# Performance work log

Hardware: AMD Instinct MI355X
Metric: run time of the kernel (lower is better)

## Reference

```python
import jax, jax.numpy as jnp
import numpy as np

DIM = 2048
NH = 16
NKV = 4
HD = DIM // NH  # 128
ROPE_BASE = 10000.0
QK_GAIN_INIT = 1.0


def setup_inputs() -> dict:
    key = jax.random.key(0)
    ks = jax.random.split(key, 6)
    kv_dim = NKV * HD
    s = 0.02
    return {
        "x": jax.random.normal(ks[0], (2, 2048, DIM), dtype=jnp.float32),
        "wq": jax.random.normal(ks[1], (DIM, DIM), dtype=jnp.float32) * s,
        "wk": jax.random.normal(ks[2], (kv_dim, DIM), dtype=jnp.float32) * s,
        "wv": jax.random.normal(ks[3], (kv_dim, DIM), dtype=jnp.float32) * s,
        "wproj": jax.random.normal(ks[4], (DIM, DIM), dtype=jnp.float32) * s,
        "q_gain": jnp.full((NH,), QK_GAIN_INIT, dtype=jnp.float32),
    }


def _rms_norm(t):
    eps = jnp.asarray(jnp.finfo(t.dtype).eps, t.dtype)
    ms = jnp.mean(jnp.square(t), axis=-1, keepdims=True)
    return t * jax.lax.rsqrt(ms + eps)


def _rope_tables(seqlen, dtype):
    inv_freq = 1.0 / (ROPE_BASE ** (np.arange(0, HD, 2, dtype=np.float32) / HD))
    t = np.arange(seqlen, dtype=np.float32)
    freqs = np.outer(t, inv_freq)  # [S, HD/2]
    cos = jnp.asarray(np.cos(freqs), dtype=dtype)[None, None]  # [1,1,S,HD/2]
    sin = jnp.asarray(np.sin(freqs), dtype=dtype)[None, None]
    return cos, sin


def _apply_rotary(x, cos, sin):
    half = x.shape[-1] // 2
    x1, x2 = x[..., :half], x[..., half:]
    return jnp.concatenate((x1 * cos + x2 * sin, -x1 * sin + x2 * cos), axis=-1)


def reference(x, wq, wk, wv, wproj, q_gain):
    B, S, D = x.shape
    # projections (torch F.linear: x @ W.T), reshape to [B, H, S, HD]
    q = (x @ wq.T).reshape(B, S, NH, HD).transpose(0, 2, 1, 3)
    k = (x @ wk.T).reshape(B, S, NKV, HD).transpose(0, 2, 1, 3)
    v = (x @ wv.T).reshape(B, S, NKV, HD).transpose(0, 2, 1, 3)
    q = _rms_norm(q)
    k = _rms_norm(k)
    cos, sin = _rope_tables(S, q.dtype)
    q = _apply_rotary(q, cos, sin)
    k = _apply_rotary(k, cos, sin)
    q = q * q_gain.astype(q.dtype)[None, :, None, None]
    # GQA: expand kv heads
    G = NH // NKV
    k = jnp.repeat(k, G, axis=1)  # [B, NH, S, HD]
    v = jnp.repeat(v, G, axis=1)
    scale = 1.0 / np.sqrt(HD)
    scores = jnp.einsum("bhsd,bhtd->bhst", q, k) * scale
    causal = jnp.tril(jnp.ones((S, S), dtype=bool))
    scores = jnp.where(causal[None, None], scores, jnp.finfo(scores.dtype).min)
    attn = jax.nn.softmax(scores, axis=-1)
    y = jnp.einsum("bhst,bhtd->bhsd", attn, v)
    y = y.transpose(0, 2, 1, 3).reshape(B, S, D)
    return y @ wproj.T
```

## Files before the change

kernel.cpp:

```cpp
#include <hip/hip_runtime.h>
#include <hip/hip_bf16.h>
#include <stdint.h>

#define DIM 2048
#define NH 16
#define NKV 4
#define HD 128
#define BATCH 2
#define SEQ 2048

typedef unsigned short ushort_t;
typedef __attribute__((ext_vector_type(8))) short short8;
typedef __attribute__((ext_vector_type(4))) float f32x4;
typedef __attribute__((ext_vector_type(16))) float f32x16;

__device__ inline ushort_t f2b(float f) {
    union { float f; uint32_t u; } v; v.f = f;
    uint32_t r = (v.u + 0x7fffu + ((v.u >> 16) & 1u)) >> 16;
    return (ushort_t)r;
}

__device__ inline float fexp2(float x) {
#if __has_builtin(__builtin_amdgcn_exp2f)
    return __builtin_amdgcn_exp2f(x);
#else
    float r; asm("v_exp_f32 %0, %1" : "=v"(r) : "v"(x)); return r;
#endif
}

__global__ void cast_all(const float* __restrict__ x, const float* __restrict__ wq,
                         const float* __restrict__ wk, const float* __restrict__ wv,
                         const float* __restrict__ wp,
                         ushort_t* __restrict__ xb, ushort_t* __restrict__ wqkvb,
                         ushort_t* __restrict__ wprojb) {
    const int stride = gridDim.x * blockDim.x;
    for (int i = blockIdx.x * blockDim.x + threadIdx.x; i < 4718592; i += stride) {
        const float* s; ushort_t* d; int off;
        if (i < 2097152)      { s = x;  d = xb;               off = i; }
        else if (i < 3145728) { s = wq; d = wqkvb;            off = i - 2097152; }
        else if (i < 3407872) { s = wk; d = wqkvb + 4194304;  off = i - 3145728; }
        else if (i < 3670016) { s = wv; d = wqkvb + 5242880;  off = i - 3407872; }
        else                  { s = wp; d = wprojb;           off = i - 3670016; }
        float4 v = ((const float4*)s)[off];
        ushort4 o;
        o.x = f2b(v.x); o.y = f2b(v.y); o.z = f2b(v.z); o.w = f2b(v.w);
        ((ushort4*)d)[off] = o;
    }
}

__device__ inline void gload_lds16(const ushort_t* g, ushort_t* l) {
    __builtin_amdgcn_global_load_lds((const __attribute__((address_space(1))) void*)g,
                                     (__attribute__((address_space(3))) void*)l, 16, 0, 0);
}

__launch_bounds__(256, 2)
__global__ void gemm_bt(const ushort_t* __restrict__ A, const ushort_t* __restrict__ Bm,
                        float* __restrict__ C, int M, int N, int K) {
    __shared__ ushort_t lA[128 * 64];
    __shared__ ushort_t lB[128 * 64];
    const int t = threadIdx.x;
    const int lane = t & 63;
    const int w = t >> 6;
    const int wr = w >> 1, wc = w & 1;
    const int g = lane >> 4, l16 = lane & 15;
    const int nwg = gridDim.x * gridDim.y;
    const int bid = blockIdx.y * gridDim.x + blockIdx.x;
    const int cpx = nwg >> 3;
    const int swz = (bid & 7) * cpx + (bid >> 3);
    const int nbx = gridDim.x;
    const int m0 = (swz / nbx) * 128, n0 = (swz % nbx) * 128;

    f32x4 acc[4][4];
#pragma unroll
    for (int i = 0; i < 4; i++)
#pragma unroll
        for (int j = 0; j < 4; j++) acc[i][j] = (f32x4){0, 0, 0, 0};

    const int row_s = t >> 3;
    const int cx = t & 7;
    const int xr = (lane & 7);

    for (int kt = 0; kt < (K >> 6); ++kt) {
        const int k0 = kt * 64;
        __syncthreads();
#pragma unroll
        for (int i = 0; i < 4; i++) {
            const int ra = i * 32 + row_s;
            gload_lds16(A + (size_t)(m0 + ra) * K + k0 + ((cx ^ (row_s & 7)) * 8), lA + i * 2048 + t * 8);
            gload_lds16(Bm + (size_t)(n0 + ra) * K + k0 + ((cx ^ (row_s & 7)) * 8), lB + i * 2048 + t * 8);
        }
        __syncthreads();
#pragma unroll
        for (int kk = 0; kk < 2; kk++) {
            short8 af[4], bf[4];
#pragma unroll
            for (int i = 0; i < 4; i++) {
                af[i] = *(const short8*)(lA + (wr * 64 + i * 16 + l16) * 64 + (((kk * 4 + g) ^ xr) * 8));
                bf[i] = *(const short8*)(lB + (wc * 64 + i * 16 + l16) * 64 + (((kk * 4 + g) ^ xr) * 8));
            }
#pragma unroll
            for (int i = 0; i < 4; i++)
#pragma unroll
                for (int j = 0; j < 4; j++)
                    acc[i][j] = __builtin_amdgcn_mfma_f32_16x16x32_bf16(af[i], bf[j], acc[i][j], 0, 0, 0);
        }
    }
#pragma unroll
    for (int i = 0; i < 4; i++)
#pragma unroll
        for (int j = 0; j < 4; j++) {
            int rb = m0 + wr * 64 + i * 16 + g * 4;
            int cb = n0 + wc * 64 + j * 16 + l16;
#pragma unroll
            for (int r = 0; r < 4; r++)
                C[(size_t)(rb + r) * N + cb] = acc[i][j][r];
        }
}

__launch_bounds__(256, 2)
__global__ void gemm_qkv(const ushort_t* __restrict__ A, const ushort_t* __restrict__ Bm,
                         const float* __restrict__ qgain,
                         ushort_t* __restrict__ qb, ushort_t* __restrict__ kb,
                         ushort_t* __restrict__ vtb) {
    const int K = 2048;
    __shared__ ushort_t lA[128 * 64];
    __shared__ ushort_t lB[128 * 64];
    __shared__ float psum[2][128];
    const int t = threadIdx.x;
    const int lane = t & 63;
    const int w = t >> 6;
    const int wr = w >> 1, wc = w & 1;
    const int g = lane >> 4, l16 = lane & 15;
    const int nwg = gridDim.x * gridDim.y;
    const int bid = blockIdx.y * gridDim.x + blockIdx.x;
    const int cpx = nwg >> 3;
    const int swz = (bid & 7) * cpx + (bid >> 3);
    const int nt = swz % 24;
    const int m0 = (swz / 24) * 128, n0 = nt * 128;

    int cm[4];
    cm[0] = wc * 32 + l16;
    cm[1] = wc * 32 + 16 + l16;
    cm[2] = cm[0] + 64;
    cm[3] = cm[1] + 64;

    f32x4 acc[4][4];
#pragma unroll
    for (int i = 0; i < 4; i++)
#pragma unroll
        for (int j = 0; j < 4; j++) acc[i][j] = (f32x4){0, 0, 0, 0};

    const int row_s = t >> 3;
    const int cx = t & 7;
    const int xr = (lane & 7);

    for (int kt = 0; kt < (K >> 6); ++kt) {
        const int k0 = kt * 64;
        __syncthreads();
#pragma unroll
        for (int i = 0; i < 4; i++) {
            const int ra = i * 32 + row_s;
            gload_lds16(A + (size_t)(m0 + ra) * K + k0 + ((cx ^ (row_s & 7)) * 8), lA + i * 2048 + t * 8);
            gload_lds16(Bm + (size_t)(n0 + ra) * K + k0 + ((cx ^ (row_s & 7)) * 8), lB + i * 2048 + t * 8);
        }
        __syncthreads();
#pragma unroll
        for (int kk = 0; kk < 2; kk++) {
            short8 af[4], bf[4];
#pragma unroll
            for (int i = 0; i < 4; i++) {
                af[i] = *(const short8*)(lA + (wr * 64 + i * 16 + l16) * 64 + (((kk * 4 + g) ^ xr) * 8));
                bf[i] = *(const short8*)(lB + cm[i] * 64 + (((kk * 4 + g) ^ xr) * 8));
            }
#pragma unroll
            for (int i = 0; i < 4; i++)
#pragma unroll
                for (int j = 0; j < 4; j++)
                    acc[i][j] = __builtin_amdgcn_mfma_f32_16x16x32_bf16(af[i], bf[j], acc[i][j], 0, 0, 0);
        }
    }

    const int b = m0 >> 11;
    const int s0 = m0 & 2047;

    if (nt < 20) {
        float ssq[4][4];
#pragma unroll
        for (int i = 0; i < 4; i++)
#pragma unroll
            for (int r = 0; r < 4; r++) {
                float v = 0.0f;
#pragma unroll
                for (int j = 0; j < 4; j++) v += acc[i][j][r] * acc[i][j][r];
#pragma unroll
                for (int m = 1; m < 16; m <<= 1) v += __shfl_xor(v, m, 64);
                ssq[i][r] = v;
            }
        if (l16 == 0) {
#pragma unroll
            for (int i = 0; i < 4; i++)
#pragma unroll
                for (int r = 0; r < 4; r++)
                    psum[wc][wr * 64 + i * 16 + g * 4 + r] = ssq[i][r];
        }
        __syncthreads();

        const float gsc = (nt < 16) ? qgain[nt] * (0.08838834764831845f * 1.4426950408889634f)
                                    : 1.0f;
        ushort_t* outp = (nt < 16) ? qb + (size_t)(b * NH + nt) * SEQ * HD
                                   : kb + (size_t)(b * NKV + (nt - 16)) * SEQ * HD;
        const float inv0 = exp2f(-(float)cm[0] * (13.287712379549449f / 64.0f));
        const float inv1 = exp2f(-(float)cm[1] * (13.287712379549449f / 64.0f));
#pragma unroll
        for (int i = 0; i < 4; i++)
#pragma unroll
            for (int r = 0; r < 4; r++) {
                const int sloc = wr * 64 + i * 16 + g * 4 + r;
                const float tot = psum[0][sloc] + psum[1][sloc];
                const float rg = rsqrtf(tot * (1.0f / 128.0f) + 1.1920929e-07f) * gsc;
                const float fs = (float)(s0 + sloc);
                ushort_t* orow = outp + (size_t)(s0 + sloc) * HD;
#pragma unroll
                for (int jp = 0; jp < 2; jp++) {
                    float x1 = acc[i][jp][r], x2 = acc[i][jp + 2][r];
                    float sn, c;
                    __sincosf(fs * (jp ? inv1 : inv0), &sn, &c);
                    orow[cm[jp]]      = f2b((x1 * c + x2 * sn) * rg);
                    orow[cm[jp] + 64] = f2b((x2 * c - x1 * sn) * rg);
                }
            }
    } else {
        ushort_t* vout = vtb + (size_t)((b * NKV + (nt - 20)) * HD) * SEQ;
#pragma unroll
        for (int i = 0; i < 4; i++)
#pragma unroll
            for (int j = 0; j < 4; j++) {
                ushort4 o;
                o.x = f2b(acc[i][j][0]); o.y = f2b(acc[i][j][1]);
                o.z = f2b(acc[i][j][2]); o.w = f2b(acc[i][j][3]);
                *(ushort4*)(vout + (size_t)cm[j] * SEQ + s0 + wr * 64 + i * 16 + g * 4) = o;
            }
    }
}

#define KVB 64

__launch_bounds__(256, 2)
__global__ void attn(const ushort_t* __restrict__ qbuf, const ushort_t* __restrict__ kbuf,
                     const ushort_t* __restrict__ vtbuf, ushort_t* __restrict__ ybuf) {
    __shared__ ushort_t Klds[KVB * HD];
    __shared__ ushort_t Vlds[HD * KVB];

    const int idx = blockIdx.x;
    const int pass = idx >> 8;
    const int rr0 = idx & 255;
    const int xcd = rr0 & 7;
    const int jj = rr0 >> 5;
    const int qt = pass ? jj : 15 - jj;
    const int bh = xcd * 4 + ((rr0 >> 3) & 3);
    const int b = bh >> 4, hh = bh & 15;
    const int kvh = hh >> 2;
    const int t = threadIdx.x;
    const int w = t >> 6, lane = t & 63;
    const int l31 = lane & 31, hf = lane >> 5;
    const int q0 = qt * 128;
    const int qbase = q0 + w * 32;

    const ushort_t* Qp = qbuf + (size_t)(b * NH + hh) * SEQ * HD;
    const ushort_t* Kp = kbuf + (size_t)(b * NKV + kvh) * SEQ * HD;
    const ushort_t* Vtp = vtbuf + (size_t)(b * NKV + kvh) * HD * SEQ;

    short8 aq[8];
#pragma unroll
    for (int dc = 0; dc < 8; dc++)
        aq[dc] = *(const short8*)(Qp + (size_t)(qbase + l31) * HD + dc * 16 + hf * 8);

    f32x16 y[4];
#pragma unroll
    for (int db = 0; db < 4; db++)
#pragma unroll
        for (int r = 0; r < 16; r++) y[db][r] = 0.0f;
    float mrun = -1e30f, lrun = 0.0f;

    const int k_row = t >> 2;
    const int k_c0 = (t & 3) * 4;
    const int v_row = t >> 1;
    const int v_c0 = (t & 1) * 4;

    short8 kreg[4], vreg[4];
    const int ntiles = q0 / 64 + 2;

#pragma unroll
    for (int i = 0; i < 4; i++) {
        kreg[i] = *(const short8*)(Kp + (size_t)k_row * HD + (k_c0 + i) * 8);
        vreg[i] = *(const short8*)(Vtp + (size_t)v_row * SEQ + (v_c0 + i) * 8);
    }

    for (int kt = 0; kt < ntiles; ++kt) {
        const int kv0 = kt * KVB;
        __syncthreads();
        {
            ushort_t* kd = Klds + k_row * HD;
            ushort_t* vd = Vlds + v_row * KVB;
#pragma unroll
            for (int i = 0; i < 4; i++)
                *(short8*)(kd + (((k_c0 + i) ^ (k_row & 15)) * 8)) = kreg[i];
#pragma unroll
            for (int i = 0; i < 4; i++)
                *(short8*)(vd + (((v_c0 + i) ^ (v_row & 7)) * 8)) = vreg[i];
        }
        __syncthreads();
        if (kt + 1 < ntiles) {
            const int nkv0 = kv0 + KVB;
#pragma unroll
            for (int i = 0; i < 4; i++) {
                kreg[i] = *(const short8*)(Kp + (size_t)(nkv0 + k_row) * HD + (k_c0 + i) * 8);
                vreg[i] = *(const short8*)(Vtp + (size_t)v_row * SEQ + nkv0 + (v_c0 + i) * 8);
            }
        }

        if (kv0 <= qbase + 31) {
            f32x16 s0v, s1v;
#pragma unroll
            for (int r = 0; r < 16; r++) { s0v[r] = 0.0f; s1v[r] = 0.0f; }
#pragma unroll
            for (int dc = 0; dc < 8; dc++) {
                short8 ak0 = *(const short8*)(Klds + (size_t)(l31) * HD      + (((dc * 2 + hf) ^ (l31 & 15)) * 8));
                short8 ak1 = *(const short8*)(Klds + (size_t)(32 + l31) * HD + (((dc * 2 + hf) ^ (l31 & 15)) * 8));
                s0v = __builtin_amdgcn_mfma_f32_32x32x16_bf16(ak0, aq[dc], s0v, 0, 0, 0);
                s1v = __builtin_amdgcn_mfma_f32_32x32x16_bf16(ak1, aq[dc], s1v, 0, 0, 0);
            }

            const int qabs = qbase + l31;
            if (kv0 + 63 > qbase) {
#pragma unroll
                for (int r = 0; r < 16; r++) {
                    int kvr = kv0 + (r & 3) + 8 * (r >> 2) + 4 * hf;
                    if (kvr > qabs)      s0v[r] = -1e30f;
                    if (kvr + 32 > qabs) s1v[r] = -1e30f;
                }
            }

            float mt = -1e30f;
#pragma unroll
            for (int r = 0; r < 16; r++) mt = fmaxf(mt, fmaxf(s0v[r], s1v[r]));
            mt = fmaxf(mt, __shfl_xor(mt, 32, 64));
            if (!__all(mt <= mrun + 8.0f)) {
                float mn = fmaxf(mrun, mt);
                float al = fexp2(mrun - mn);
                mrun = mn;
                lrun *= al;
#pragma unroll
                for (int r = 0; r < 16; r++) {
                    float alr = __shfl(al, (r & 3) + 8 * (r >> 2) + 4 * hf, 64);
#pragma unroll
                    for (int db = 0; db < 4; db++) y[db][r] *= alr;
                }
            }
            float sum = 0.0f;
#pragma unroll
            for (int r = 0; r < 16; r++) {
                float p0 = fexp2(s0v[r] - mrun);
                float p1 = fexp2(s1v[r] - mrun);
                s0v[r] = p0; s1v[r] = p1;
                sum += p0 + p1;
            }
            sum += __shfl_xor(sum, 32, 64);
            lrun += sum;

            union PW { short8 v; uint32_t wd[4]; } pa[4];
#pragma unroll
            for (int blk = 0; blk < 2; blk++) {
#pragma unroll
                for (int ks2 = 0; ks2 < 2; ks2++) {
#pragma unroll
                    for (int t2 = 0; t2 < 2; t2++) {
                        float a0 = blk ? s1v[8 * ks2 + 2 * t2]         : s0v[8 * ks2 + 2 * t2];
                        float a1 = blk ? s1v[8 * ks2 + 2 * t2 + 1]     : s0v[8 * ks2 + 2 * t2 + 1];
                        float b0 = blk ? s1v[8 * ks2 + 4 + 2 * t2]     : s0v[8 * ks2 + 4 + 2 * t2];
                        float b1 = blk ? s1v[8 * ks2 + 4 + 2 * t2 + 1] : s0v[8 * ks2 + 4 + 2 * t2 + 1];
                        uint32_t pw = (uint32_t)f2b(a0) | ((uint32_t)f2b(a1) << 16);
                        uint32_t qw = (uint32_t)f2b(b0) | ((uint32_t)f2b(b1) << 16);
                        uint32_t send = hf ? pw : qw;
                        uint32_t recv = (uint32_t)__shfl_xor((int)send, 32, 64);
                        pa[blk * 2 + ks2].wd[t2]     = hf ? recv : pw;
                        pa[blk * 2 + ks2].wd[t2 + 2] = hf ? qw : recv;
                    }
                }
            }

#pragma unroll
            for (int ks = 0; ks < 4; ks++) {
#pragma unroll
                for (int db = 0; db < 4; db++) {
                    short8 bv = *(const short8*)(Vlds + (size_t)(db * 32 + l31) * KVB
                                                 + (((ks * 2 + hf) ^ (l31 & 7)) * 8));
                    y[db] = __builtin_amdgcn_mfma_f32_32x32x16_bf16(pa[ks].v, bv, y[db], 0, 0, 0);
                }
            }
        }
    }

    float linv = 1.0f / lrun;
    ushort_t* Yp = ybuf + (size_t)b * SEQ * DIM + hh * HD;
#pragma unroll
    for (int r = 0; r < 16; r++) {
        int qloc = (r & 3) + 8 * (r >> 2) + 4 * hf;
        float lr = __shfl(linv, qloc, 64);
        int q = qbase + qloc;
#pragma unroll
        for (int db = 0; db < 4; db++)
            Yp[(size_t)q * DIM + db * 32 + l31] = f2b(y[db][r] * lr);
    }
}

extern "C" void kernel_launch(void* const* d_in, const int* in_sizes, int n_in,
                              void* d_out, int out_size, void* d_ws, size_t ws_size,
                              hipStream_t stream) {
    (void)in_sizes; (void)n_in; (void)out_size; (void)ws_size;
    const float* x     = (const float*)d_in[0];
    const float* wq    = (const float*)d_in[1];
    const float* wk    = (const float*)d_in[2];
    const float* wv    = (const float*)d_in[3];
    const float* wproj = (const float*)d_in[4];
    const float* qg    = (const float*)d_in[5];

    char* ws = (char*)d_ws;
    ushort_t* xb     = (ushort_t*)ws;
    ushort_t* wqkvb  = (ushort_t*)(ws + (16u << 20));
    ushort_t* wprojb = (ushort_t*)(ws + (28u << 20));
    ushort_t* qb     = (ushort_t*)(ws + (36u << 20));
    ushort_t* kb     = (ushort_t*)(ws + (52u << 20));
    ushort_t* vtb    = (ushort_t*)(ws + (56u << 20));
    ushort_t* yb     = (ushort_t*)(ws + (60u << 20));

    cast_all<<<2048, 256, 0, stream>>>(x, wq, wk, wv, wproj, xb, wqkvb, wprojb);
    gemm_qkv<<<dim3(24, 32), 256, 0, stream>>>(xb, wqkvb, qg, qb, kb, vtb);
    attn<<<512, 256, 0, stream>>>(qb, kb, vtb, yb);
    gemm_bt<<<dim3(16, 32), 256, 0, stream>>>(yb, wprojb, (float*)d_out, 4096, 2048, 2048);
}
```

Baseline: 174.4 us.

## Double-buffer K/V tiles in attention LDS and use packed bf16 convert

The attention kernel now keeps two K/V tiles in LDS. It writes tile kt+1 while computing on tile kt and prefetches tile kt+2 into registers, so there is one barrier per iteration instead of two. The manual round-to-nearest bf16 packing of probabilities is replaced with the hardware v_cvt_pk_bf16_f32 instruction. Doubling LDS to 64KB per block may limit occupancy at the declared two blocks per CU.

```diff
diff --git a/kernel.cpp b/kernel.cpp
--- a/kernel.cpp
+++ b/kernel.cpp
@@ -26,6 +26,12 @@
 #else
     float r; asm("v_exp_f32 %0, %1" : "=v"(r) : "v"(x)); return r;
 #endif
+}
+
+__device__ inline uint32_t pk2bf(float a, float b) {
+    uint32_t r;
+    asm("v_cvt_pk_bf16_f32 %0, %1, %2" : "=v"(r) : "v"(a), "v"(b));
+    return r;
 }
 
 __global__ void cast_all(const float* __restrict__ x, const float* __restrict__ wq,
@@ -248,8 +254,8 @@
 __launch_bounds__(256, 2)
 __global__ void attn(const ushort_t* __restrict__ qbuf, const ushort_t* __restrict__ kbuf,
                      const ushort_t* __restrict__ vtbuf, ushort_t* __restrict__ ybuf) {
-    __shared__ ushort_t Klds[KVB * HD];
-    __shared__ ushort_t Vlds[HD * KVB];
+    __shared__ ushort_t Klds[2][KVB * HD];
+    __shared__ ushort_t Vlds[2][HD * KVB];
 
     const int idx = blockIdx.x;
     const int pass = idx >> 8;
@@ -295,13 +301,30 @@
         kreg[i] = *(const short8*)(Kp + (size_t)k_row * HD + (k_c0 + i) * 8);
         vreg[i] = *(const short8*)(Vtp + (size_t)v_row * SEQ + (v_c0 + i) * 8);
     }
+    {
+        ushort_t* kd = Klds[0] + k_row * HD;
+        ushort_t* vd = Vlds[0] + v_row * KVB;
+#pragma unroll
+        for (int i = 0; i < 4; i++)
+            *(short8*)(kd + (((k_c0 + i) ^ (k_row & 15)) * 8)) = kreg[i];
+#pragma unroll
+        for (int i = 0; i < 4; i++)
+            *(short8*)(vd + (((v_c0 + i) ^ (v_row & 7)) * 8)) = vreg[i];
+    }
+    if (ntiles > 1) {
+#pragma unroll
+        for (int i = 0; i < 4; i++) {
+            kreg[i] = *(const short8*)(Kp + (size_t)(KVB + k_row) * HD + (k_c0 + i) * 8);
+            vreg[i] = *(const short8*)(Vtp + (size_t)v_row * SEQ + KVB + (v_c0 + i) * 8);
+        }
+    }
+    __syncthreads();
 
     for (int kt = 0; kt < ntiles; ++kt) {
         const int kv0 = kt * KVB;
-        __syncthreads();
-        {
-            ushort_t* kd = Klds + k_row * HD;
-            ushort_t* vd = Vlds + v_row * KVB;
+        if (kt + 1 < ntiles) {
+            ushort_t* kd = Klds[(kt + 1) & 1] + k_row * HD;
+            ushort_t* vd = Vlds[(kt + 1) & 1] + v_row * KVB;
 #pragma unroll
             for (int i = 0; i < 4; i++)
                 *(short8*)(kd + (((k_c0 + i) ^ (k_row & 15)) * 8)) = kreg[i];
@@ -309,9 +332,8 @@
             for (int i = 0; i < 4; i++)
                 *(short8*)(vd + (((v_c0 + i) ^ (v_row & 7)) * 8)) = vreg[i];
         }
-        __syncthreads();
-        if (kt + 1 < ntiles) {
-            const int nkv0 = kv0 + KVB;
+        if (kt + 2 < ntiles) {
+            const int nkv0 = kv0 + 2 * KVB;
 #pragma unroll
             for (int i = 0; i < 4; i++) {
                 kreg[i] = *(const short8*)(Kp + (size_t)(nkv0 + k_row) * HD + (k_c0 + i) * 8);
@@ -320,13 +342,16 @@
         }
 
         if (kv0 <= qbase + 31) {
+            const ushort_t* Kl = Klds[kt & 1];
+            const ushort_t* Vl = Vlds[kt & 1];
+
             f32x16 s0v, s1v;
 #pragma unroll
             for (int r = 0; r < 16; r++) { s0v[r] = 0.0f; s1v[r] = 0.0f; }
 #pragma unroll
             for (int dc = 0; dc < 8; dc++) {
-                short8 ak0 = *(const short8*)(Klds + (size_t)(l31) * HD      + (((dc * 2 + hf) ^ (l31 & 15)) * 8));
-                short8 ak1 = *(const short8*)(Klds + (size_t)(32 + l31) * HD + (((dc * 2 + hf) ^ (l31 & 15)) * 8));
+                short8 ak0 = *(const short8*)(Kl + (size_t)(l31) * HD      + (((dc * 2 + hf) ^ (l31 & 15)) * 8));
+                short8 ak1 = *(const short8*)(Kl + (size_t)(32 + l31) * HD + (((dc * 2 + hf) ^ (l31 & 15)) * 8));
                 s0v = __builtin_amdgcn_mfma_f32_32x32x16_bf16(ak0, aq[dc], s0v, 0, 0, 0);
                 s1v = __builtin_amdgcn_mfma_f32_32x32x16_bf16(ak1, aq[dc], s1v, 0, 0, 0);
             }
@@ -379,8 +404,8 @@
                         float a1 = blk ? s1v[8 * ks2 + 2 * t2 + 1]     : s0v[8 * ks2 + 2 * t2 + 1];
                         float b0 = blk ? s1v[8 * ks2 + 4 + 2 * t2]     : s0v[8 * ks2 + 4 + 2 * t2];
                         float b1 = blk ? s1v[8 * ks2 + 4 + 2 * t2 + 1] : s0v[8 * ks2 + 4 + 2 * t2 + 1];
-                        uint32_t pw = (uint32_t)f2b(a0) | ((uint32_t)f2b(a1) << 16);
-                        uint32_t qw = (uint32_t)f2b(b0) | ((uint32_t)f2b(b1) << 16);
+                        uint32_t pw = pk2bf(a0, a1);
+                        uint32_t qw = pk2bf(b0, b1);
                         uint32_t send = hf ? pw : qw;
                         uint32_t recv = (uint32_t)__shfl_xor((int)send, 32, 64);
                         pa[blk * 2 + ks2].wd[t2]     = hf ? recv : pw;
@@ -393,12 +418,13 @@
             for (int ks = 0; ks < 4; ks++) {
 #pragma unroll
                 for (int db = 0; db < 4; db++) {
-                    short8 bv = *(const short8*)(Vlds + (size_t)(db * 32 + l31) * KVB
+                    short8 bv = *(const short8*)(Vl + (size_t)(db * 32 + l31) * KVB
                                                  + (((ks * 2 + hf) ^ (l31 & 7)) * 8));
                     y[db] = __builtin_amdgcn_mfma_f32_32x32x16_bf16(pa[ks].v, bv, y[db], 0, 0, 0);
                 }
             }
         }
+        __syncthreads();
     }
 
     float linv = 1.0f / lrun;
```

After: 171.0 us (median of 4 runs). Within noise of the previous version (-1.9%).
